# Optimization experiments

Measured on AMD Instinct MI355X. Metric: run time of the kernel, lower is better.

The kernel has to match this reference:

```python
import jax, jax.numpy as jnp
import numpy as np

N = 100000  # number of nodes
SELF_LOOP_W = 2.0  # improved=True in PyG GCNConv


def gcn_conv(x, edge_index, W, b):
    # x: [N, Fin], edge_index: [2, E] (row=src, col=dst), W: [Fin, Fout], b: [Fout]
    src, dst = edge_index[0], edge_index[1]
    h = x @ W  # [N, Fout]
    # degree with improved self-loops (weight 2.0)
    ones = jnp.ones(src.shape, dtype=h.dtype)
    deg = jax.ops.segment_sum(ones, dst, num_segments=N) + SELF_LOOP_W
    dinv = jnp.where(deg > 0, jax.lax.rsqrt(deg), 0.0)
    norm = dinv[src] * dinv[dst]  # [E]
    agg = jax.ops.segment_sum(h[src] * norm[:, None], dst, num_segments=N)
    # self-loop contribution: weight 2.0, norm = dinv_i * 2 * dinv_i
    agg = agg + h * (SELF_LOOP_W * dinv * dinv)[:, None]
    return agg + b


def setup_inputs() -> dict:
    key = jax.random.key(0)
    ks = jax.random.split(key, 6)
    x = jax.random.normal(ks[0], (N, 64), dtype=jnp.float32)
    edge_index = jax.random.randint(ks[1], (2, 1600000), 0, N, dtype=jnp.int64)
    W1 = jax.random.normal(ks[2], (64, 64), dtype=jnp.float32) * 0.1
    b1 = jax.random.normal(ks[3], (64,), dtype=jnp.float32) * 0.1
    W2 = jax.random.normal(ks[4], (64, 32), dtype=jnp.float32) * 0.1
    b2 = jax.random.normal(ks[5], (32,), dtype=jnp.float32) * 0.1
    return {"x": x, "edge_index": edge_index, "W1": W1, "b1": b1, "W2": W2, "b2": b2}


def reference(x, edge_index, W1, b1, W2, b2):
    h1 = jax.nn.relu(gcn_conv(x, edge_index, W1, b1))
    feature_map = h1
    out = gcn_conv(h1, edge_index, W2, b2)
    return (out, feature_map)
```

## Files before the change

kernel.cpp:

```cpp
#include <hip/hip_runtime.h>

#define N_NODES 100000
#define E_EDGES 1600000

#define BSHIFT 7
#define BSIZE 128
#define NBUCK ((N_NODES + BSIZE - 1) / BSIZE)
#define STAGE_TPB 512
#define STAGE_EPT 8
#define STAGE_CHUNK (STAGE_TPB * STAGE_EPT)
#define NREP 2
#define BUCKET_CAP 4096

typedef __attribute__((ext_vector_type(8))) short short8;
typedef __attribute__((ext_vector_type(4))) float float4v;

__device__ inline unsigned short f2bf(float f) {
    union { float f; unsigned u; } t; t.f = f;
    unsigned r = (t.u + 0x7fffu + ((t.u >> 16) & 1u)) >> 16;
    return (unsigned short)r;
}
__device__ inline float bf2f(unsigned short h) {
    union { unsigned u; float f; } t; t.u = ((unsigned)h) << 16; return t.f;
}
__device__ inline unsigned pack_bf16x2(float a, float b) {
    return (unsigned)f2bf(a) | ((unsigned)f2bf(b) << 16);
}
__device__ inline float bf_lo(unsigned u) { union { unsigned u; float f; } t; t.u = u << 16; return t.f; }
__device__ inline float bf_hi(unsigned u) { union { unsigned u; float f; } t; t.u = u & 0xffff0000u; return t.f; }

__global__ void cursor_init_kernel(int* __restrict__ gcursor) {
    int b = blockIdx.x * blockDim.x + threadIdx.x;
    if (b < NBUCK) gcursor[b] = b * BUCKET_CAP;
}

__global__ void __launch_bounds__(STAGE_TPB) stage_kernel(
    const int* __restrict__ src, const int* __restrict__ dst,
    int* __restrict__ gcursor, unsigned* __restrict__ staged, int E) {
    __shared__ int hist[NREP][NBUCK];
    __shared__ int base[NREP][NBUCK];
    const int tid = threadIdx.x;
    const int rep = (tid >> 8) & (NREP - 1);
    const int e0 = blockIdx.x * STAGE_CHUNK;
    for (int i = tid; i < NREP * NBUCK; i += STAGE_TPB) ((int*)hist)[i] = 0;
    __syncthreads();
    int d[STAGE_EPT], s[STAGE_EPT];
#pragma unroll
    for (int k = 0; k < STAGE_EPT; ++k) {
        int e = e0 + k * STAGE_TPB + tid;
        if (e < E) {
            d[k] = dst[e];
            s[k] = src[e];
            atomicAdd(&hist[rep][d[k] >> BSHIFT], 1);
        } else {
            d[k] = -1;
        }
    }
    __syncthreads();
    for (int i = tid; i < NBUCK; i += STAGE_TPB) {
        int h0 = hist[0][i], h1 = hist[1][i];
        int t = h0 + h1;
        if (t > 0) {
            int g = atomicAdd(&gcursor[i], t);
            base[0][i] = g;
            base[1][i] = g + h0;
        }
    }
    __syncthreads();
#pragma unroll
    for (int k = 0; k < STAGE_EPT; ++k) {
        if (d[k] >= 0) {
            int b = d[k] >> BSHIFT;
            int pos = atomicAdd(&base[rep][b], 1);
            if (pos < (b + 1) * BUCKET_CAP)
                staged[pos] = (unsigned)s[k] | ((unsigned)(d[k] & (BSIZE - 1)) << 17);
        }
    }
}

__global__ void bscan_kernel(const int* __restrict__ gcursor, int* __restrict__ boff) {
    __shared__ int s[1024];
    const int tid = threadIdx.x;
    int v = 0;
    if (tid < NBUCK) {
        v = gcursor[tid] - tid * BUCKET_CAP;
        if (v > BUCKET_CAP) v = BUCKET_CAP;
    }
    s[tid] = v;
    __syncthreads();
    for (int off = 1; off < 1024; off <<= 1) {
        int t = (tid >= off) ? s[tid - off] : 0;
        __syncthreads();
        s[tid] += t;
        __syncthreads();
    }
    if (tid < NBUCK) boff[tid] = s[tid] - v;
    if (tid == NBUCK - 1) boff[NBUCK] = s[tid];
}

__global__ void bucket_csr_kernel(const unsigned* __restrict__ staged,
                                  const int* __restrict__ boff,
                                  int2* __restrict__ nodeinfo, float* __restrict__ dinv,
                                  int* __restrict__ csrc, int n) {
    __shared__ int ldeg[BSIZE];
    __shared__ int lrp[BSIZE];
    __shared__ int lcnt[BSIZE];
    __shared__ unsigned lrec[BUCKET_CAP];
    __shared__ int lsrc[BUCKET_CAP];
    const int b = blockIdx.x;
    const int node0 = b * BSIZE;
    const int nn = min(BSIZE, n - node0);
    const int tid = threadIdx.x;
    if (tid < BSIZE) { ldeg[tid] = 0; lcnt[tid] = 0; }
    __syncthreads();
    const int ebase = boff[b];
    const int ecnt = min(boff[b + 1] - ebase, BUCKET_CAP);
    const int sbase = b * BUCKET_CAP;
    for (int i = tid; i < ecnt; i += 256) {
        unsigned r = staged[sbase + i];
        lrec[i] = r;
        atomicAdd(&ldeg[r >> 17], 1);
    }
    __syncthreads();
    int mydeg = (tid < BSIZE) ? ldeg[tid] : 0;
    if (tid < BSIZE) lrp[tid] = mydeg;
    __syncthreads();
    for (int off = 1; off < BSIZE; off <<= 1) {
        int v = 0;
        if (tid < BSIZE && tid >= off) v = lrp[tid - off];
        __syncthreads();
        if (tid < BSIZE) lrp[tid] += v;
        __syncthreads();
    }
    if (tid < BSIZE) {
        int ex = lrp[tid] - mydeg;
        lrp[tid] = ex;
        if (tid < nn) {
            nodeinfo[node0 + tid] = make_int2(ebase + ex, mydeg);
            dinv[node0 + tid] = rsqrtf((float)mydeg + 2.0f);
        }
    }
    __syncthreads();
    for (int i = tid; i < ecnt; i += 256) {
        unsigned r = lrec[i];
        int dl = (int)(r >> 17);
        int sv = (int)(r & 0x1FFFFu);
        int pos = lrp[dl] + atomicAdd(&lcnt[dl], 1);
        if (pos < BUCKET_CAP) lsrc[pos] = sv;
    }
    __syncthreads();
    for (int i = tid; i < ecnt; i += 256)
        csrc[ebase + i] = lsrc[i];
}

template <int FOUT>
__global__ void __launch_bounds__(256) linear_mfma_kernel(
    const float* __restrict__ X, const float* __restrict__ W,
    const float* __restrict__ dinv, unsigned* __restrict__ HS, int n) {
    constexpr int NT = FOUT / 16;
    const int NTILES_M = n / 16;
    const int lane = threadIdx.x & 63;
    const int gwave = blockIdx.x * 4 + (threadIdx.x >> 6);
    const int nwaves = gridDim.x * 4;
    const int m = lane & 15;
    const int q = lane >> 4;

    short8 Bhi[2][NT], Blo[2][NT];
#pragma unroll
    for (int ks = 0; ks < 2; ++ks)
#pragma unroll
        for (int nt = 0; nt < NT; ++nt) {
            short8 bh, bl;
#pragma unroll
            for (int j = 0; j < 8; ++j) {
                int k = ks * 32 + q * 8 + j;
                float wv = W[k * FOUT + nt * 16 + m];
                unsigned short h = f2bf(wv);
                bh[j] = (short)h;
                bl[j] = (short)f2bf(wv - bf2f(h));
            }
            Bhi[ks][nt] = bh;
            Blo[ks][nt] = bl;
        }

    for (int tile = gwave; tile < NTILES_M; tile += nwaves) {
        const int row0 = tile * 16;
        float4v C[NT];
#pragma unroll
        for (int nt = 0; nt < NT; ++nt) C[nt] = (float4v){0.f, 0.f, 0.f, 0.f};
#pragma unroll
        for (int ks = 0; ks < 2; ++ks) {
            const float* xp = X + (size_t)(row0 + m) * 64 + ks * 32 + q * 8;
            float4v x0 = *(const float4v*)xp;
            float4v x1 = *(const float4v*)(xp + 4);
            short8 Ahi, Alo;
#pragma unroll
            for (int j = 0; j < 4; ++j) {
                unsigned short h0 = f2bf(x0[j]);
                Ahi[j] = (short)h0;
                Alo[j] = (short)f2bf(x0[j] - bf2f(h0));
                unsigned short h1 = f2bf(x1[j]);
                Ahi[4 + j] = (short)h1;
                Alo[4 + j] = (short)f2bf(x1[j] - bf2f(h1));
            }
#pragma unroll
            for (int nt = 0; nt < NT; ++nt) {
                C[nt] = __builtin_amdgcn_mfma_f32_16x16x32_bf16(Ahi, Bhi[ks][nt], C[nt], 0, 0, 0);
                C[nt] = __builtin_amdgcn_mfma_f32_16x16x32_bf16(Alo, Bhi[ks][nt], C[nt], 0, 0, 0);
                C[nt] = __builtin_amdgcn_mfma_f32_16x16x32_bf16(Ahi, Blo[ks][nt], C[nt], 0, 0, 0);
            }
        }
#pragma unroll
        for (int ch = 0; ch < NT / 2; ++ch) {
#pragma unroll
            for (int reg = 0; reg < 4; ++reg) {
                int r = row0 + q * 4 + reg;
                float di = dinv[r];
                unsigned u = pack_bf16x2(C[2 * ch][reg] * di, C[2 * ch + 1][reg] * di);
                HS[(size_t)ch * n * 16 + (size_t)r * 16 + m] = u;
            }
        }
    }
}

template <int NCHUNK, bool RELU>
__global__ void gather_chunk_kernel(const int2* __restrict__ nodeinfo,
                                    const int* __restrict__ csrc, const unsigned* __restrict__ HS0,
                                    const float* __restrict__ dinv, const float* __restrict__ bias,
                                    float* __restrict__ OUT, int n) {
    constexpr int G = 16;
    constexpr int NPB = 256 / G;
    const int chunk = blockIdx.x & (NCHUNK - 1);
    int node = (blockIdx.x / NCHUNK) * NPB + (threadIdx.x / G);
    int l = threadIdx.x % G;
    if (node >= n) return;
    const unsigned* __restrict__ HS = HS0 + (size_t)chunk * n * G;
    const float* __restrict__ bias0 = bias + 32 * chunk;
    const int out_stride = 32 * NCHUNK;
    const int out_off = 32 * chunk;
    int2 ni = nodeinfo[node];
    int start = ni.x, cnt = ni.y;
    unsigned us = HS[(size_t)node * G + l];
    float a0 = 2.0f * bf_lo(us);
    float a1 = 2.0f * bf_hi(us);
    float b0 = 0.0f, b1 = 0.0f;
    int j = start, end = start + cnt;
    for (; j + 7 < end; j += 8) {
        int s0 = csrc[j],     s1 = csrc[j + 1], s2 = csrc[j + 2], s3 = csrc[j + 3];
        int s4 = csrc[j + 4], s5 = csrc[j + 5], s6 = csrc[j + 6], s7 = csrc[j + 7];
        unsigned u0 = HS[(size_t)s0 * G + l];
        unsigned u1 = HS[(size_t)s1 * G + l];
        unsigned u2 = HS[(size_t)s2 * G + l];
        unsigned u3 = HS[(size_t)s3 * G + l];
        unsigned u4 = HS[(size_t)s4 * G + l];
        unsigned u5 = HS[(size_t)s5 * G + l];
        unsigned u6 = HS[(size_t)s6 * G + l];
        unsigned u7 = HS[(size_t)s7 * G + l];
        a0 += bf_lo(u0) + bf_lo(u1) + bf_lo(u2) + bf_lo(u3);
        a1 += bf_hi(u0) + bf_hi(u1) + bf_hi(u2) + bf_hi(u3);
        b0 += bf_lo(u4) + bf_lo(u5) + bf_lo(u6) + bf_lo(u7);
        b1 += bf_hi(u4) + bf_hi(u5) + bf_hi(u6) + bf_hi(u7);
    }
    for (; j + 3 < end; j += 4) {
        int s0 = csrc[j], s1 = csrc[j + 1], s2 = csrc[j + 2], s3 = csrc[j + 3];
        unsigned u0 = HS[(size_t)s0 * G + l];
        unsigned u1 = HS[(size_t)s1 * G + l];
        unsigned u2 = HS[(size_t)s2 * G + l];
        unsigned u3 = HS[(size_t)s3 * G + l];
        a0 += bf_lo(u0) + bf_lo(u1);
        a1 += bf_hi(u0) + bf_hi(u1);
        b0 += bf_lo(u2) + bf_lo(u3);
        b1 += bf_hi(u2) + bf_hi(u3);
    }
    for (; j < end; ++j) {
        unsigned u = HS[(size_t)csrc[j] * G + l];
        a0 += bf_lo(u);
        a1 += bf_hi(u);
    }
    a0 += b0;
    a1 += b1;
    float dd = dinv[node];
    float o0 = a0 * dd + bias0[l];
    float o1 = a1 * dd + bias0[16 + l];
    if (RELU) { o0 = fmaxf(o0, 0.0f); o1 = fmaxf(o1, 0.0f); }
    OUT[(size_t)node * out_stride + out_off + l] = o0;
    OUT[(size_t)node * out_stride + out_off + 16 + l] = o1;
}

extern "C" void kernel_launch(void* const* d_in, const int* in_sizes, int n_in,
                              void* d_out, int out_size, void* d_ws, size_t ws_size,
                              hipStream_t stream) {
    const float* x  = (const float*)d_in[0];
    const int*   ei = (const int*)d_in[1];
    const float* W1 = (const float*)d_in[2];
    const float* b1 = (const float*)d_in[3];
    const float* W2 = (const float*)d_in[4];
    const float* b2 = (const float*)d_in[5];

    const int* srcp = ei;
    const int* dstp = ei + E_EDGES;

    float* out = (float*)d_out;
    float* fm  = (float*)d_out + N_NODES * 32;

    char* w = (char*)d_ws;
    int*      gcursor  = (int*)w;       w += sizeof(int) * NBUCK;
    int*      boff     = (int*)w;       w += sizeof(int) * (NBUCK + 1);
    int2*     nodeinfo = (int2*)w;      w += sizeof(int2) * N_NODES;
    float*    dinv     = (float*)w;     w += sizeof(float) * N_NODES;
    int*      csrc     = (int*)w;       w += sizeof(int) * E_EDGES;
    unsigned* staged   = (unsigned*)w;  w += sizeof(unsigned) * (size_t)NBUCK * BUCKET_CAP;
    unsigned* HS1      = (unsigned*)w;  w += sizeof(unsigned) * (size_t)N_NODES * 32;
    unsigned* HS2      = (unsigned*)w;  w += sizeof(unsigned) * (size_t)N_NODES * 16;

    cursor_init_kernel<<<(NBUCK + 255) / 256, 256, 0, stream>>>(gcursor);
    stage_kernel<<<(E_EDGES + STAGE_CHUNK - 1) / STAGE_CHUNK, STAGE_TPB, 0, stream>>>(
        srcp, dstp, gcursor, staged, E_EDGES);
    bscan_kernel<<<1, 1024, 0, stream>>>(gcursor, boff);
    bucket_csr_kernel<<<NBUCK, 256, 0, stream>>>(staged, boff, nodeinfo, dinv, csrc, N_NODES);

    linear_mfma_kernel<64><<<512, 256, 0, stream>>>(x, W1, dinv, HS1, N_NODES);
    gather_chunk_kernel<2, true><<<2 * ((N_NODES + 15) / 16), 256, 0, stream>>>(
        nodeinfo, csrc, HS1, dinv, b1, fm, N_NODES);

    linear_mfma_kernel<32><<<512, 256, 0, stream>>>(fm, W2, dinv, HS2, N_NODES);
    gather_chunk_kernel<1, false><<<(N_NODES + 15) / 16, 256, 0, stream>>>(
        nodeinfo, csrc, HS2, dinv, b2, out, N_NODES);
}
```

Measured before the change: 217.2 us.

## Pad CSR rows to multiples of four and gather features with 128-bit vector loads

```diff
diff --git a/kernel.cpp b/kernel.cpp
--- a/kernel.cpp
+++ b/kernel.cpp
@@ -14,6 +14,8 @@
 
 typedef __attribute__((ext_vector_type(8))) short short8;
 typedef __attribute__((ext_vector_type(4))) float float4v;
+typedef __attribute__((ext_vector_type(4))) int int4v;
+typedef __attribute__((ext_vector_type(4))) unsigned uint4v;
 
 __device__ inline unsigned short f2bf(float f) {
     union { float f; unsigned u; } t; t.f = f;
@@ -29,9 +31,12 @@
 __device__ inline float bf_lo(unsigned u) { union { unsigned u; float f; } t; t.u = u << 16; return t.f; }
 __device__ inline float bf_hi(unsigned u) { union { unsigned u; float f; } t; t.u = u & 0xffff0000u; return t.f; }
 
-__global__ void cursor_init_kernel(int* __restrict__ gcursor) {
+__global__ void cursor_init_kernel(int* __restrict__ gcursor,
+                                   unsigned* __restrict__ HS1, unsigned* __restrict__ HS2) {
     int b = blockIdx.x * blockDim.x + threadIdx.x;
     if (b < NBUCK) gcursor[b] = b * BUCKET_CAP;
+    if (b < 32) HS1[(size_t)N_NODES * 32 + b] = 0u;
+    if (b < 16) HS2[(size_t)N_NODES * 16 + b] = 0u;
 }
 
 __global__ void __launch_bounds__(STAGE_TPB) stage_kernel(
@@ -46,14 +51,20 @@
     __syncthreads();
     int d[STAGE_EPT], s[STAGE_EPT];
 #pragma unroll
-    for (int k = 0; k < STAGE_EPT; ++k) {
-        int e = e0 + k * STAGE_TPB + tid;
+    for (int k = 0; k < STAGE_EPT / 4; ++k) {
+        int e = e0 + (k * STAGE_TPB + tid) * 4;
         if (e < E) {
-            d[k] = dst[e];
-            s[k] = src[e];
-            atomicAdd(&hist[rep][d[k] >> BSHIFT], 1);
+            int4v sv = *(const int4v*)(src + e);
+            int4v dv = *(const int4v*)(dst + e);
+#pragma unroll
+            for (int i = 0; i < 4; ++i) {
+                s[4 * k + i] = sv[i];
+                d[4 * k + i] = dv[i];
+                atomicAdd(&hist[rep][dv[i] >> BSHIFT], 1);
+            }
         } else {
-            d[k] = -1;
+#pragma unroll
+            for (int i = 0; i < 4; ++i) d[4 * k + i] = -1;
         }
     }
     __syncthreads();
@@ -85,6 +96,7 @@
     if (tid < NBUCK) {
         v = gcursor[tid] - tid * BUCKET_CAP;
         if (v > BUCKET_CAP) v = BUCKET_CAP;
+        v = (v + 391) & ~3;
     }
     s[tid] = v;
     __syncthreads();
@@ -99,14 +111,17 @@
 }
 
 __global__ void bucket_csr_kernel(const unsigned* __restrict__ staged,
+                                  const int* __restrict__ gcursor,
                                   const int* __restrict__ boff,
                                   int2* __restrict__ nodeinfo, float* __restrict__ dinv,
                                   int* __restrict__ csrc, int n) {
     __shared__ int ldeg[BSIZE];
-    __shared__ int lrp[BSIZE];
+    __shared__ int laex[BSIZE];
+    __shared__ int lscan[BSIZE];
     __shared__ int lcnt[BSIZE];
     __shared__ unsigned lrec[BUCKET_CAP];
-    __shared__ int lsrc[BUCKET_CAP];
+    __shared__ int lsrc[BUCKET_CAP + 512];
+    __shared__ int ltot;
     const int b = blockIdx.x;
     const int node0 = b * BSIZE;
     const int nn = min(BSIZE, n - node0);
@@ -114,7 +129,8 @@
     if (tid < BSIZE) { ldeg[tid] = 0; lcnt[tid] = 0; }
     __syncthreads();
     const int ebase = boff[b];
-    const int ecnt = min(boff[b + 1] - ebase, BUCKET_CAP);
+    int ecnt = gcursor[b] - b * BUCKET_CAP;
+    if (ecnt > BUCKET_CAP) ecnt = BUCKET_CAP;
     const int sbase = b * BUCKET_CAP;
     for (int i = tid; i < ecnt; i += 256) {
         unsigned r = staged[sbase + i];
@@ -123,21 +139,24 @@
     }
     __syncthreads();
     int mydeg = (tid < BSIZE) ? ldeg[tid] : 0;
-    if (tid < BSIZE) lrp[tid] = mydeg;
+    int adeg = (mydeg + 3) & ~3;
+    if (tid < BSIZE) lscan[tid] = adeg;
     __syncthreads();
     for (int off = 1; off < BSIZE; off <<= 1) {
         int v = 0;
-        if (tid < BSIZE && tid >= off) v = lrp[tid - off];
+        if (tid < BSIZE && tid >= off) v = lscan[tid - off];
         __syncthreads();
-        if (tid < BSIZE) lrp[tid] += v;
+        if (tid < BSIZE) lscan[tid] += v;
         __syncthreads();
     }
     if (tid < BSIZE) {
-        int ex = lrp[tid] - mydeg;
-        lrp[tid] = ex;
+        int aex = lscan[tid] - adeg;
+        laex[tid] = aex;
+        if (tid == BSIZE - 1) ltot = lscan[tid];
         if (tid < nn) {
-            nodeinfo[node0 + tid] = make_int2(ebase + ex, mydeg);
+            nodeinfo[node0 + tid] = make_int2(ebase + aex, mydeg);
             dinv[node0 + tid] = rsqrtf((float)mydeg + 2.0f);
+            for (int k = mydeg; k < adeg; ++k) lsrc[aex + k] = N_NODES;
         }
     }
     __syncthreads();
@@ -145,11 +164,12 @@
         unsigned r = lrec[i];
         int dl = (int)(r >> 17);
         int sv = (int)(r & 0x1FFFFu);
-        int pos = lrp[dl] + atomicAdd(&lcnt[dl], 1);
-        if (pos < BUCKET_CAP) lsrc[pos] = sv;
-    }
-    __syncthreads();
-    for (int i = tid; i < ecnt; i += 256)
+        int pos = laex[dl] + atomicAdd(&lcnt[dl], 1);
+        if (pos < BUCKET_CAP + 512) lsrc[pos] = sv;
+    }
+    __syncthreads();
+    const int tot = ltot;
+    for (int i = tid; i < tot; i += 256)
         csrc[ebase + i] = lsrc[i];
 }
 
@@ -158,6 +178,7 @@
     const float* __restrict__ X, const float* __restrict__ W,
     const float* __restrict__ dinv, unsigned* __restrict__ HS, int n) {
     constexpr int NT = FOUT / 16;
+    constexpr int ROWU = NT * 8;
     const int NTILES_M = n / 16;
     const int lane = threadIdx.x & 63;
     const int gwave = blockIdx.x * 4 + (threadIdx.x >> 6);
@@ -217,74 +238,87 @@
                 int r = row0 + q * 4 + reg;
                 float di = dinv[r];
                 unsigned u = pack_bf16x2(C[2 * ch][reg] * di, C[2 * ch + 1][reg] * di);
-                HS[(size_t)ch * n * 16 + (size_t)r * 16 + m] = u;
-            }
-        }
-    }
-}
-
-template <int NCHUNK, bool RELU>
-__global__ void gather_chunk_kernel(const int2* __restrict__ nodeinfo,
-                                    const int* __restrict__ csrc, const unsigned* __restrict__ HS0,
-                                    const float* __restrict__ dinv, const float* __restrict__ bias,
-                                    float* __restrict__ OUT, int n) {
-    constexpr int G = 16;
+                HS[(size_t)r * ROWU + ch * 16 + m] = u;
+            }
+        }
+    }
+}
+
+template <int ROWU, bool RELU>
+__global__ void __launch_bounds__(256) gather_vec_kernel(
+    const int2* __restrict__ nodeinfo, const int* __restrict__ csrc,
+    const unsigned* __restrict__ HS, const float* __restrict__ dinv,
+    const float* __restrict__ bias, float* __restrict__ OUT, int n) {
+    constexpr int G = ROWU / 4;
     constexpr int NPB = 256 / G;
-    const int chunk = blockIdx.x & (NCHUNK - 1);
-    int node = (blockIdx.x / NCHUNK) * NPB + (threadIdx.x / G);
-    int l = threadIdx.x % G;
+    constexpr int FOUT = ROWU * 2;
+    const int node = blockIdx.x * NPB + (int)(threadIdx.x / G);
+    const int t = threadIdx.x % G;
     if (node >= n) return;
-    const unsigned* __restrict__ HS = HS0 + (size_t)chunk * n * G;
-    const float* __restrict__ bias0 = bias + 32 * chunk;
-    const int out_stride = 32 * NCHUNK;
-    const int out_off = 32 * chunk;
     int2 ni = nodeinfo[node];
-    int start = ni.x, cnt = ni.y;
-    unsigned us = HS[(size_t)node * G + l];
-    float a0 = 2.0f * bf_lo(us);
-    float a1 = 2.0f * bf_hi(us);
-    float b0 = 0.0f, b1 = 0.0f;
-    int j = start, end = start + cnt;
-    for (; j + 7 < end; j += 8) {
-        int s0 = csrc[j],     s1 = csrc[j + 1], s2 = csrc[j + 2], s3 = csrc[j + 3];
-        int s4 = csrc[j + 4], s5 = csrc[j + 5], s6 = csrc[j + 6], s7 = csrc[j + 7];
-        unsigned u0 = HS[(size_t)s0 * G + l];
-        unsigned u1 = HS[(size_t)s1 * G + l];
-        unsigned u2 = HS[(size_t)s2 * G + l];
-        unsigned u3 = HS[(size_t)s3 * G + l];
-        unsigned u4 = HS[(size_t)s4 * G + l];
-        unsigned u5 = HS[(size_t)s5 * G + l];
-        unsigned u6 = HS[(size_t)s6 * G + l];
-        unsigned u7 = HS[(size_t)s7 * G + l];
-        a0 += bf_lo(u0) + bf_lo(u1) + bf_lo(u2) + bf_lo(u3);
-        a1 += bf_hi(u0) + bf_hi(u1) + bf_hi(u2) + bf_hi(u3);
-        b0 += bf_lo(u4) + bf_lo(u5) + bf_lo(u6) + bf_lo(u7);
-        b1 += bf_hi(u4) + bf_hi(u5) + bf_hi(u6) + bf_hi(u7);
-    }
-    for (; j + 3 < end; j += 4) {
-        int s0 = csrc[j], s1 = csrc[j + 1], s2 = csrc[j + 2], s3 = csrc[j + 3];
-        unsigned u0 = HS[(size_t)s0 * G + l];
-        unsigned u1 = HS[(size_t)s1 * G + l];
-        unsigned u2 = HS[(size_t)s2 * G + l];
-        unsigned u3 = HS[(size_t)s3 * G + l];
-        a0 += bf_lo(u0) + bf_lo(u1);
-        a1 += bf_hi(u0) + bf_hi(u1);
-        b0 += bf_lo(u2) + bf_lo(u3);
-        b1 += bf_hi(u2) + bf_hi(u3);
-    }
-    for (; j < end; ++j) {
-        unsigned u = HS[(size_t)csrc[j] * G + l];
-        a0 += bf_lo(u);
-        a1 += bf_hi(u);
-    }
-    a0 += b0;
-    a1 += b1;
-    float dd = dinv[node];
-    float o0 = a0 * dd + bias0[l];
-    float o1 = a1 * dd + bias0[16 + l];
-    if (RELU) { o0 = fmaxf(o0, 0.0f); o1 = fmaxf(o1, 0.0f); }
-    OUT[(size_t)node * out_stride + out_off + l] = o0;
-    OUT[(size_t)node * out_stride + out_off + 16 + l] = o1;
+    const int start = ni.x;
+    const int deg = ni.y;
+    const int pend = start + ((deg + 3) & ~3);
+    const unsigned* __restrict__ HSt = HS + 4 * t;
+    const uint4v own = *(const uint4v*)(HS + (size_t)node * ROWU + 4 * t);
+    float alo[4], ahi[4];
+#pragma unroll
+    for (int k = 0; k < 4; ++k) { alo[k] = 2.0f * bf_lo(own[k]); ahi[k] = 2.0f * bf_hi(own[k]); }
+    int j = start;
+    for (; j + 8 <= pend; j += 8) {
+        int4v s0 = *(const int4v*)(csrc + j);
+        int4v s1 = *(const int4v*)(csrc + j + 4);
+        uint4v u0 = *(const uint4v*)(HSt + (size_t)s0[0] * ROWU);
+        uint4v u1 = *(const uint4v*)(HSt + (size_t)s0[1] * ROWU);
+        uint4v u2 = *(const uint4v*)(HSt + (size_t)s0[2] * ROWU);
+        uint4v u3 = *(const uint4v*)(HSt + (size_t)s0[3] * ROWU);
+        uint4v u4 = *(const uint4v*)(HSt + (size_t)s1[0] * ROWU);
+        uint4v u5 = *(const uint4v*)(HSt + (size_t)s1[1] * ROWU);
+        uint4v u6 = *(const uint4v*)(HSt + (size_t)s1[2] * ROWU);
+        uint4v u7 = *(const uint4v*)(HSt + (size_t)s1[3] * ROWU);
+#pragma unroll
+        for (int k = 0; k < 4; ++k) {
+            float l01 = bf_lo(u0[k]) + bf_lo(u1[k]);
+            float l23 = bf_lo(u2[k]) + bf_lo(u3[k]);
+            float l45 = bf_lo(u4[k]) + bf_lo(u5[k]);
+            float l67 = bf_lo(u6[k]) + bf_lo(u7[k]);
+            alo[k] += (l01 + l23) + (l45 + l67);
+            float h01 = bf_hi(u0[k]) + bf_hi(u1[k]);
+            float h23 = bf_hi(u2[k]) + bf_hi(u3[k]);
+            float h45 = bf_hi(u4[k]) + bf_hi(u5[k]);
+            float h67 = bf_hi(u6[k]) + bf_hi(u7[k]);
+            ahi[k] += (h01 + h23) + (h45 + h67);
+        }
+    }
+    if (j < pend) {
+        int4v s0 = *(const int4v*)(csrc + j);
+        uint4v u0 = *(const uint4v*)(HSt + (size_t)s0[0] * ROWU);
+        uint4v u1 = *(const uint4v*)(HSt + (size_t)s0[1] * ROWU);
+        uint4v u2 = *(const uint4v*)(HSt + (size_t)s0[2] * ROWU);
+        uint4v u3 = *(const uint4v*)(HSt + (size_t)s0[3] * ROWU);
+#pragma unroll
+        for (int k = 0; k < 4; ++k) {
+            alo[k] += (bf_lo(u0[k]) + bf_lo(u1[k])) + (bf_lo(u2[k]) + bf_lo(u3[k]));
+            ahi[k] += (bf_hi(u0[k]) + bf_hi(u1[k])) + (bf_hi(u2[k]) + bf_hi(u3[k]));
+        }
+    }
+    const float dd = dinv[node];
+    const int ch = t >> 2;
+    const int c0 = (4 * t) & 15;
+    const float4v blv = *(const float4v*)(bias + 32 * ch + c0);
+    const float4v bhv = *(const float4v*)(bias + 32 * ch + 16 + c0);
+    float4v olo, ohi;
+#pragma unroll
+    for (int k = 0; k < 4; ++k) {
+        float o0 = alo[k] * dd + blv[k];
+        float o1 = ahi[k] * dd + bhv[k];
+        if (RELU) { o0 = fmaxf(o0, 0.0f); o1 = fmaxf(o1, 0.0f); }
+        olo[k] = o0;
+        ohi[k] = o1;
+    }
+    float* op = OUT + (size_t)node * FOUT + 32 * ch + c0;
+    *(float4v*)op = olo;
+    *(float4v*)(op + 16) = ohi;
 }
 
 extern "C" void kernel_launch(void* const* d_in, const int* in_sizes, int n_in,
@@ -308,22 +342,22 @@
     int*      boff     = (int*)w;       w += sizeof(int) * (NBUCK + 1);
     int2*     nodeinfo = (int2*)w;      w += sizeof(int2) * N_NODES;
     float*    dinv     = (float*)w;     w += sizeof(float) * N_NODES;
-    int*      csrc     = (int*)w;       w += sizeof(int) * E_EDGES;
+    int*      csrc     = (int*)w;       w += sizeof(int) * (E_EDGES + NBUCK * 392);
     unsigned* staged   = (unsigned*)w;  w += sizeof(unsigned) * (size_t)NBUCK * BUCKET_CAP;
-    unsigned* HS1      = (unsigned*)w;  w += sizeof(unsigned) * (size_t)N_NODES * 32;
-    unsigned* HS2      = (unsigned*)w;  w += sizeof(unsigned) * (size_t)N_NODES * 16;
-
-    cursor_init_kernel<<<(NBUCK + 255) / 256, 256, 0, stream>>>(gcursor);
+    unsigned* HS1      = (unsigned*)w;  w += sizeof(unsigned) * (size_t)(N_NODES + 1) * 32;
+    unsigned* HS2      = (unsigned*)w;  w += sizeof(unsigned) * (size_t)(N_NODES + 1) * 16;
+
+    cursor_init_kernel<<<(NBUCK + 255) / 256, 256, 0, stream>>>(gcursor, HS1, HS2);
     stage_kernel<<<(E_EDGES + STAGE_CHUNK - 1) / STAGE_CHUNK, STAGE_TPB, 0, stream>>>(
         srcp, dstp, gcursor, staged, E_EDGES);
     bscan_kernel<<<1, 1024, 0, stream>>>(gcursor, boff);
-    bucket_csr_kernel<<<NBUCK, 256, 0, stream>>>(staged, boff, nodeinfo, dinv, csrc, N_NODES);
+    bucket_csr_kernel<<<NBUCK, 256, 0, stream>>>(staged, gcursor, boff, nodeinfo, dinv, csrc, N_NODES);
 
     linear_mfma_kernel<64><<<512, 256, 0, stream>>>(x, W1, dinv, HS1, N_NODES);
-    gather_chunk_kernel<2, true><<<2 * ((N_NODES + 15) / 16), 256, 0, stream>>>(
+    gather_vec_kernel<32, true><<<(N_NODES + 31) / 32, 256, 0, stream>>>(
         nodeinfo, csrc, HS1, dinv, b1, fm, N_NODES);
 
     linear_mfma_kernel<32><<<512, 256, 0, stream>>>(fm, W2, dinv, HS2, N_NODES);
-    gather_chunk_kernel<1, false><<<(N_NODES + 15) / 16, 256, 0, stream>>>(
+    gather_vec_kernel<16, false><<<(N_NODES + 63) / 64, 256, 0, stream>>>(
         nodeinfo, csrc, HS2, dinv, b2, out, N_NODES);
 }
```

New measurement: 213.0 us. Within noise of the previous version (-1.9%).
